# Kernel tuning notes

Measured on AMD Instinct MI355X. Metric: run time of the kernel, lower is better.

The kernel has to match this reference:

```python
import jax, jax.numpy as jnp
import numpy as np

B, T = 1024, 128
LEN_VOCAB, IPD_VOCAB = 1500, 256
LEN_EB, IPD_EB = 64, 64
RNN_IN, HIDDEN, LABELS = 128, 512, 100


def setup_inputs() -> dict:
    key = jax.random.key(0)
    ks = jax.random.split(key, 11)
    std = 1.0 / np.sqrt(HIDDEN)

    def u(k, shape, s):
        return jax.random.uniform(k, shape, jnp.float32, -s, s)

    return {
        "x": jax.random.randint(ks[0], (B, T, 2), 0, 256, dtype=jnp.int64),
        "len_emb": jax.random.normal(ks[1], (LEN_VOCAB, LEN_EB), jnp.float32),
        "ipd_emb": jax.random.normal(ks[2], (IPD_VOCAB, IPD_EB), jnp.float32),
        "fc1_w": u(ks[3], (RNN_IN, LEN_EB + IPD_EB), 1.0 / np.sqrt(LEN_EB + IPD_EB)),
        "fc1_b": u(ks[4], (RNN_IN,), 1.0 / np.sqrt(LEN_EB + IPD_EB)),
        "x2h_w": u(ks[5], (HIDDEN, RNN_IN), std),
        "x2h_b": u(ks[6], (HIDDEN,), std),
        "h2h_w": u(ks[7], (HIDDEN, HIDDEN), std),
        "h2h_b": u(ks[8], (HIDDEN,), std),
        "fc2_w": u(ks[9], (LABELS, HIDDEN), 1.0 / np.sqrt(HIDDEN)),
        "fc2_b": u(ks[10], (LABELS,), 1.0 / np.sqrt(HIDDEN)),
    }


def reference(x, len_emb, ipd_emb, fc1_w, fc1_b, x2h_w, x2h_b, h2h_w, h2h_b, fc2_w, fc2_b):
    # Embedding lookups: [B, T, 64] each -> concat [B, T, 128]
    feats = jnp.concatenate([len_emb[x[:, :, 0]], ipd_emb[x[:, :, 1]]], axis=-1)
    # fc1 then precompute the x2h part of the recurrence for all timesteps
    r = feats @ fc1_w.T + fc1_b                       # [B, T, RNN_IN]
    xin = r @ x2h_w.T + x2h_b                         # [B, T, HIDDEN]
    xin_t = jnp.swapaxes(xin, 0, 1)                   # [T, B, HIDDEN]

    def step(h, xt):
        h = jnp.tanh(xt + h @ h2h_w.T + h2h_b)
        return h, None

    h0 = jnp.zeros((x.shape[0], h2h_w.shape[0]), dtype=xin.dtype)
    h_last, _ = jax.lax.scan(step, h0, xin_t)
    # eval mode: dropout is identity
    return h_last @ fc2_w.T + fc2_b                   # [B, LABELS]
```

## Files before the change

### kernel.cpp

```cpp
#include <hip/hip_runtime.h>

#define B_SZ 1024
#define T_SZ 128
#define HID 512
#define LAB 100

#define OFF_XC    0u
#define OFF_WH    262144u
#define OFF_FC2   786432u
#define OFF_FC2B  888832u
#define OFF_WEFFT 889344u
#define OFF_BEFF  1151488u
#define OFF_ELEN  1153536u
#define OFF_EIPD  1415680u
#define WS_NEED   1677824u

typedef __attribute__((ext_vector_type(8))) short short8;
typedef __attribute__((ext_vector_type(8))) unsigned short us8;
typedef __attribute__((ext_vector_type(4))) float float4v;
typedef __attribute__((ext_vector_type(4))) unsigned short us4;
typedef __attribute__((ext_vector_type(8))) __bf16 bf8_t;
typedef unsigned long long ull;

__device__ __attribute__((aligned(16))) unsigned char g_blob[WS_NEED];

__device__ __forceinline__ float bf2f(unsigned short u) {
    union { unsigned int i; float f; } z; z.i = ((unsigned int)u) << 16; return z.f;
}
__device__ __forceinline__ unsigned short f2bf(float f) {
    union { float f; unsigned int i; } z; z.f = f;
    unsigned int r = z.i + 0x7FFFu + ((z.i >> 16) & 1u);
    return (unsigned short)(r >> 16);
}
__device__ __forceinline__ float4v mfma16(short8 a, short8 b, float4v c) {
    return __builtin_amdgcn_mfma_f32_16x16x32_bf16(
        __builtin_bit_cast(bf8_t, a), __builtin_bit_cast(bf8_t, b), c, 0, 0, 0);
}

__launch_bounds__(256)
__global__ void k1_kernel(const float* __restrict__ fc1_f, const float* __restrict__ fc1b_f,
                          const float* __restrict__ x2h_f, const float* __restrict__ x2hb_f,
                          const float* __restrict__ h2hb_f,
                          float* __restrict__ wefft, float* __restrict__ beff) {
    const int tid = threadIdx.x;
    if (blockIdx.x < 64) {
        int gid = blockIdx.x * 256 + tid;
        int n  = gid >> 5;
        int k0 = (gid & 31) * 4;
        const float* xr = x2h_f + n * 128;
        float a0 = 0.f, a1 = 0.f, a2 = 0.f, a3 = 0.f;
#pragma unroll 4
        for (int j = 0; j < 128; j++) {
            float xv = xr[j];
            float4v fv = *(const float4v*)(fc1_f + j * 128 + k0);
            a0 += xv * fv[0]; a1 += xv * fv[1];
            a2 += xv * fv[2]; a3 += xv * fv[3];
        }
        wefft[(k0 + 0) * 512 + n] = a0;
        wefft[(k0 + 1) * 512 + n] = a1;
        wefft[(k0 + 2) * 512 + n] = a2;
        wefft[(k0 + 3) * 512 + n] = a3;
        return;
    }
    int tg = (blockIdx.x - 64) * 256 + tid;
    float s = x2hb_f[tg] + h2hb_f[tg];
    const float4v* xr = (const float4v*)(x2h_f + tg * 128);
    const float4v* bb = (const float4v*)fc1b_f;
    for (int j = 0; j < 32; j++) {
        float4v a = xr[j], b = bb[j];
        s += a[0] * b[0] + a[1] * b[1] + a[2] * b[2] + a[3] * b[3];
    }
    beff[tg] = s;
}

__launch_bounds__(256)
__global__ void k2_kernel(const float* __restrict__ wefft, const float* __restrict__ beff,
                          const float* __restrict__ len_f, const float* __restrict__ ipd_f,
                          const int* __restrict__ xi, unsigned char* __restrict__ xc,
                          const float* __restrict__ h2h_f, const float* __restrict__ fc2_f,
                          const float* __restrict__ fc2b_f,
                          unsigned short* __restrict__ elen, unsigned short* __restrict__ eipd,
                          unsigned short* __restrict__ o_wh, unsigned short* __restrict__ o_fc2,
                          float* __restrict__ o_fc2b) {
    const int tid = threadIdx.x;
    if (blockIdx.x < 256) {
        int grp = blockIdx.x * 256 + tid;
        int tab = grp >> 15;
        int g2  = grp & 32767;
        int v   = g2 >> 7;
        int nq  = (g2 & 127) * 4;
        const float* emb = (tab ? ipd_f : len_f) + v * 64;
        const float* wt  = wefft + tab * 64 * 512 + nq;
        float a0 = 0.f, a1 = 0.f, a2 = 0.f, a3 = 0.f;
#pragma unroll 8
        for (int k = 0; k < 64; k++) {
            float e = emb[k];
            float4v w = *(const float4v*)(wt + k * 512);
            a0 += e * w[0]; a1 += e * w[1]; a2 += e * w[2]; a3 += e * w[3];
        }
        if (tab) {
            float4v b4 = *(const float4v*)&beff[nq];
            a0 += b4[0]; a1 += b4[1]; a2 += b4[2]; a3 += b4[3];
        }
        int nt = (nq >> 4) & 3, qq = (nq >> 2) & 3;
        int p0 = (nq & ~63) + ((nt >> 1) << 5) + qq * 8 + ((nt & 1) << 2);
        us4 o = { f2bf(a0), f2bf(a1), f2bf(a2), f2bf(a3) };
        unsigned short* dst = tab ? eipd : elen;
        *(us4*)&dst[v * 512 + p0] = o;
        return;
    }
    if (blockIdx.x < 512) {
        __shared__ int is64;
        if (tid == 0) {
            int nz = 0;
            for (int j = 1; j < 64; j += 2) nz |= xi[j];
            is64 = (nz == 0) ? 1 : 0;
        }
        __syncthreads();
        const int n = B_SZ * T_SZ * 2;
        const int i64 = is64;
        for (int i = (blockIdx.x - 256) * 256 + tid; i < n; i += 256 * 256) {
            int v = i64 ? xi[2 * i] : xi[i];
            v = v < 0 ? 0 : (v > 255 ? 255 : v);
            int b = i >> 8, r = i & 255, t = r >> 1, c = r & 1;
            xc[t * 2048 + b * 2 + c] = (unsigned char)v;
        }
        return;
    }
    const int N2 = 262144, N3 = 51200, N5 = 100;
    const int total = N2 + N3 + N5;
    for (int i = (blockIdx.x - 512) * 256 + tid; i < total; i += 613 * 256) {
        int j = i;
        if (j < N2) { o_wh[j] = f2bf(h2h_f[j]); continue; }
        j -= N2;
        if (j < N3) { o_fc2[j] = f2bf(fc2_f[j]); continue; }
        j -= N3;
        o_fc2b[j] = fc2b_f[j];
    }
}

__launch_bounds__(512, 2)
__global__ void rnn_kernel(const unsigned short* __restrict__ w_wh,
                           const unsigned char* __restrict__ w_xc,
                           const unsigned short* __restrict__ w_elen,
                           const unsigned short* __restrict__ w_eipd,
                           const unsigned short* __restrict__ w_fc2,
                           const float* __restrict__ w_fc2b,
                           float* __restrict__ out) {
    extern __shared__ unsigned short sm2[];
    unsigned short* sA = sm2;
    unsigned short* sH = sm2 + 65536;

    const int tid  = threadIdx.x;
    const int wv   = tid >> 6;
    const int ln   = tid & 63;
    const int mcol = ln & 15;
    const int q    = ln >> 4;
    const int g    = blockIdx.x;
    const int b0   = g * 16;
    const int n0   = wv * 64;

    for (int it = 0; it < 16; it++) {
        int chunk = it * 512 + tid;
        int r = chunk >> 4, c = chunk & 15;
        uint4 v = *(const uint4*)(w_wh + r * 512 + 384 + c * 8);
        *(uint4*)&sA[r * 128 + ((c ^ (r & 15)) & 15) * 8] = v;
    }
    {
        uint4 z = {0, 0, 0, 0};
        *(uint4*)&sH[tid * 8] = z;
        *(uint4*)&sH[(512 + tid) * 8] = z;
    }
    short8 whr[4][12];
#pragma unroll
    for (int nt = 0; nt < 4; nt++)
#pragma unroll
        for (int kt = 0; kt < 12; kt++)
            whr[nt][kt] = *(const short8*)(w_wh + (n0 + nt * 16 + mcol) * 512 + kt * 32 + q * 8);

    const int qlo = (q ^ (mcol & 3)) * 8;
    int ej[4];
#pragma unroll
    for (int j = 0; j < 4; j++)
        ej[j] = ((j * 4) ^ (mcol & 12)) * 8;
    const int base_b = mcol * 512 + qlo;
    const int fbase  = (n0 + mcol) * 128 + qlo;
    int hw_off[4];
#pragma unroll
    for (int nt = 0; nt < 4; nt++) {
        int n = n0 + nt * 16 + q * 4;
        hw_off[nt] = mcol * 512 + (((n >> 3) ^ mcol) & 63) * 8 + (n & 7);
    }

    const int xb2  = (b0 + mcol) * 2;
    const int ecol = n0 + q * 8;
    us8 tL0, tL1, tI0, tI1;
    {
        unsigned int i0 = *(const unsigned short*)&w_xc[xb2];
        const unsigned short* eL = w_elen + (i0 & 255u) * 512 + ecol;
        const unsigned short* eI = w_eipd + (i0 >> 8) * 512 + ecol;
        tL0 = *(const us8*)eL;  tL1 = *(const us8*)(eL + 32);
        tI0 = *(const us8*)eI;  tI1 = *(const us8*)(eI + 32);
    }
    unsigned int idxP = *(const unsigned short*)&w_xc[2048 + xb2];

    __syncthreads();

    for (int t = 0; t < T_SZ; t++) {
        const unsigned short* hRd = sH + ((t & 1) << 13);
        unsigned short* hWr = sH + (((t + 1) & 1) << 13);

        float4v acc[4];
#pragma unroll
        for (int r = 0; r < 4; r++) {
            acc[0][r] = bf2f(tL0[r])     + bf2f(tI0[r]);
            acc[1][r] = bf2f(tL0[4 + r]) + bf2f(tI0[4 + r]);
            acc[2][r] = bf2f(tL1[r])     + bf2f(tI1[r]);
            acc[3][r] = bf2f(tL1[4 + r]) + bf2f(tI1[4 + r]);
        }
        if (t + 1 < T_SZ) {
            const unsigned short* eL = w_elen + (idxP & 255u) * 512 + ecol;
            const unsigned short* eI = w_eipd + (idxP >> 8) * 512 + ecol;
            tL0 = *(const us8*)eL;  tL1 = *(const us8*)(eL + 32);
            tI0 = *(const us8*)eI;  tI1 = *(const us8*)(eI + 32);
            if (t + 2 < T_SZ)
                idxP = *(const unsigned short*)&w_xc[(t + 2) * 2048 + xb2];
        }

#pragma unroll
        for (int kt = 0; kt < 12; kt++) {
            short8 bh = *(const short8*)&hRd[base_b + ej[kt & 3] + (kt >> 2) * 128];
#pragma unroll
            for (int nt = 0; nt < 4; nt++)
                acc[nt] = mfma16(whr[nt][kt], bh, acc[nt]);
        }
#pragma unroll
        for (int j = 0; j < 4; j++) {
            short8 bh = *(const short8*)&hRd[base_b + ej[j] + 384];
#pragma unroll
            for (int nt = 0; nt < 4; nt++) {
                short8 fa = *(const short8*)&sA[fbase + nt * 2048 + ej[j]];
                acc[nt] = mfma16(fa, bh, acc[nt]);
            }
        }

#pragma unroll
        for (int nt = 0; nt < 4; nt++) {
            unsigned short o[4];
#pragma unroll
            for (int r = 0; r < 4; r++) {
                float e  = __expf(2.0f * acc[nt][r]);
                float th = 1.0f - 2.0f * __builtin_amdgcn_rcpf(e + 1.0f);
                o[r] = f2bf(th);
            }
            us4 v4 = { o[0], o[1], o[2], o[3] };
            *(us4*)&hWr[hw_off[nt]] = v4;
        }
        __syncthreads();
    }

    unsigned short* hF = sH;

    if (wv < 7) {
        int lA = wv * 16 + mcol; if (lA > 99) lA = 99;
        float4v a2 = {0.f, 0.f, 0.f, 0.f};
#pragma unroll
        for (int kt = 0; kt < 16; kt++) {
            short8 fa = *(const short8*)(w_fc2 + lA * 512 + kt * 32 + q * 8);
            short8 bh = *(const short8*)&hF[base_b + ej[kt & 3] + (kt >> 2) * 128];
            a2 = mfma16(fa, bh, a2);
        }
#pragma unroll
        for (int r = 0; r < 4; r++) {
            int l = wv * 16 + q * 4 + r;
            if (l < 100) out[(b0 + mcol) * 100 + l] = a2[r] + w_fc2b[l];
        }
    }
}

extern "C" void kernel_launch(void* const* d_in, const int* in_sizes, int n_in,
                              void* d_out, int out_size, void* d_ws, size_t ws_size,
                              hipStream_t stream) {
    unsigned char* base = (unsigned char*)d_ws;
    if (ws_size < (size_t)WS_NEED) {
        void* p = nullptr;
        hipGetSymbolAddress(&p, HIP_SYMBOL(g_blob));
        base = (unsigned char*)p;
    }
    unsigned char*  w_xc    = base + OFF_XC;
    unsigned short* w_wh    = (unsigned short*)(base + OFF_WH);
    unsigned short* w_fc2   = (unsigned short*)(base + OFF_FC2);
    float*          w_fc2b  = (float*)(base + OFF_FC2B);
    float*          w_wefft = (float*)(base + OFF_WEFFT);
    float*          w_beff  = (float*)(base + OFF_BEFF);
    unsigned short* w_elen  = (unsigned short*)(base + OFF_ELEN);
    unsigned short* w_eipd  = (unsigned short*)(base + OFF_EIPD);

    static bool attr_set = false;
    if (!attr_set) {
        hipFuncSetAttribute((const void*)rnn_kernel,
                            hipFuncAttributeMaxDynamicSharedMemorySize, 163840);
        attr_set = true;
    }

    k1_kernel<<<66, 256, 0, stream>>>(
        (const float*)d_in[3], (const float*)d_in[4],
        (const float*)d_in[5], (const float*)d_in[6], (const float*)d_in[8],
        w_wefft, w_beff);
    k2_kernel<<<1125, 256, 0, stream>>>(
        w_wefft, w_beff,
        (const float*)d_in[1], (const float*)d_in[2],
        (const int*)d_in[0], w_xc,
        (const float*)d_in[7], (const float*)d_in[9], (const float*)d_in[10],
        w_elen, w_eipd, w_wh, w_fc2, w_fc2b);
    rnn_kernel<<<64, 512, 163840, stream>>>(
        w_wh, w_xc, w_elen, w_eipd, w_fc2, w_fc2b, (float*)d_out);
}
```

Before: 354.8 us.

## Fuse prep kernels with flag sync and keep more h2h weights in registers

Result: slower. 488.8 us (+37.8%).

```diff
diff --git a/kernel.cpp b/kernel.cpp
--- a/kernel.cpp
+++ b/kernel.cpp
@@ -13,7 +13,8 @@
 #define OFF_BEFF  1151488u
 #define OFF_ELEN  1153536u
 #define OFF_EIPD  1415680u
-#define WS_NEED   1677824u
+#define OFF_FLAGS 1677824u
+#define WS_NEED   1677840u
 
 typedef __attribute__((ext_vector_type(8))) short short8;
 typedef __attribute__((ext_vector_type(8))) unsigned short us8;
@@ -38,13 +39,22 @@
 }
 
 __launch_bounds__(256)
-__global__ void k1_kernel(const float* __restrict__ fc1_f, const float* __restrict__ fc1b_f,
-                          const float* __restrict__ x2h_f, const float* __restrict__ x2hb_f,
-                          const float* __restrict__ h2hb_f,
-                          float* __restrict__ wefft, float* __restrict__ beff) {
+__global__ void k12_kernel(const float* __restrict__ fc1_f, const float* __restrict__ fc1b_f,
+                           const float* __restrict__ x2h_f, const float* __restrict__ x2hb_f,
+                           const float* __restrict__ h2hb_f,
+                           const float* __restrict__ len_f, const float* __restrict__ ipd_f,
+                           const int* __restrict__ xi, unsigned char* __restrict__ xc,
+                           const float* __restrict__ h2h_f, const float* __restrict__ fc2_f,
+                           const float* __restrict__ fc2b_f,
+                           float* wefft, float* beff,
+                           unsigned short* __restrict__ elen, unsigned short* __restrict__ eipd,
+                           unsigned short* __restrict__ o_wh, unsigned short* __restrict__ o_fc2,
+                           float* __restrict__ o_fc2b,
+                           unsigned int* __restrict__ flags) {
     const int tid = threadIdx.x;
-    if (blockIdx.x < 64) {
-        int gid = blockIdx.x * 256 + tid;
+    const int b   = blockIdx.x;
+    if (b < 64) {
+        int gid = b * 256 + tid;
         int n  = gid >> 5;
         int k0 = (gid & 31) * 4;
         const float* xr = x2h_f + n * 128;
@@ -60,31 +70,38 @@
         wefft[(k0 + 1) * 512 + n] = a1;
         wefft[(k0 + 2) * 512 + n] = a2;
         wefft[(k0 + 3) * 512 + n] = a3;
+        __syncthreads();
+        if (tid == 0) {
+            __threadfence();
+            __hip_atomic_fetch_add(&flags[0], 1u, __ATOMIC_RELEASE, __HIP_MEMORY_SCOPE_SYSTEM);
+        }
         return;
     }
-    int tg = (blockIdx.x - 64) * 256 + tid;
-    float s = x2hb_f[tg] + h2hb_f[tg];
-    const float4v* xr = (const float4v*)(x2h_f + tg * 128);
-    const float4v* bb = (const float4v*)fc1b_f;
-    for (int j = 0; j < 32; j++) {
-        float4v a = xr[j], b = bb[j];
-        s += a[0] * b[0] + a[1] * b[1] + a[2] * b[2] + a[3] * b[3];
-    }
-    beff[tg] = s;
-}
-
-__launch_bounds__(256)
-__global__ void k2_kernel(const float* __restrict__ wefft, const float* __restrict__ beff,
-                          const float* __restrict__ len_f, const float* __restrict__ ipd_f,
-                          const int* __restrict__ xi, unsigned char* __restrict__ xc,
-                          const float* __restrict__ h2h_f, const float* __restrict__ fc2_f,
-                          const float* __restrict__ fc2b_f,
-                          unsigned short* __restrict__ elen, unsigned short* __restrict__ eipd,
-                          unsigned short* __restrict__ o_wh, unsigned short* __restrict__ o_fc2,
-                          float* __restrict__ o_fc2b) {
-    const int tid = threadIdx.x;
-    if (blockIdx.x < 256) {
-        int grp = blockIdx.x * 256 + tid;
+    if (b < 66) {
+        int tg = (b - 64) * 256 + tid;
+        float s = x2hb_f[tg] + h2hb_f[tg];
+        const float4v* xr = (const float4v*)(x2h_f + tg * 128);
+        const float4v* bb = (const float4v*)fc1b_f;
+        for (int j = 0; j < 32; j++) {
+            float4v a = xr[j], c = bb[j];
+            s += a[0] * c[0] + a[1] * c[1] + a[2] * c[2] + a[3] * c[3];
+        }
+        beff[tg] = s;
+        __syncthreads();
+        if (tid == 0) {
+            __threadfence();
+            __hip_atomic_fetch_add(&flags[0], 1u, __ATOMIC_RELEASE, __HIP_MEMORY_SCOPE_SYSTEM);
+        }
+        return;
+    }
+    if (b < 322) {
+        if (tid == 0) {
+            while (__hip_atomic_load(&flags[0], __ATOMIC_RELAXED, __HIP_MEMORY_SCOPE_SYSTEM) < 66u)
+                __builtin_amdgcn_s_sleep(8);
+            __threadfence();
+        }
+        __syncthreads();
+        int grp = (b - 66) * 256 + tid;
         int tab = grp >> 15;
         int g2  = grp & 32767;
         int v   = g2 >> 7;
@@ -109,7 +126,7 @@
         *(us4*)&dst[v * 512 + p0] = o;
         return;
     }
-    if (blockIdx.x < 512) {
+    if (b < 578) {
         __shared__ int is64;
         if (tid == 0) {
             int nz = 0;
@@ -119,17 +136,17 @@
         __syncthreads();
         const int n = B_SZ * T_SZ * 2;
         const int i64 = is64;
-        for (int i = (blockIdx.x - 256) * 256 + tid; i < n; i += 256 * 256) {
+        for (int i = (b - 322) * 256 + tid; i < n; i += 256 * 256) {
             int v = i64 ? xi[2 * i] : xi[i];
             v = v < 0 ? 0 : (v > 255 ? 255 : v);
-            int b = i >> 8, r = i & 255, t = r >> 1, c = r & 1;
-            xc[t * 2048 + b * 2 + c] = (unsigned char)v;
+            int bb2 = i >> 8, r = i & 255, t = r >> 1, c = r & 1;
+            xc[t * 2048 + bb2 * 2 + c] = (unsigned char)v;
         }
         return;
     }
     const int N2 = 262144, N3 = 51200, N5 = 100;
     const int total = N2 + N3 + N5;
-    for (int i = (blockIdx.x - 512) * 256 + tid; i < total; i += 613 * 256) {
+    for (int i = (b - 578) * 256 + tid; i < total; i += 613 * 256) {
         int j = i;
         if (j < N2) { o_wh[j] = f2bf(h2h_f[j]); continue; }
         j -= N2;
@@ -149,7 +166,7 @@
                            float* __restrict__ out) {
     extern __shared__ unsigned short sm2[];
     unsigned short* sA = sm2;
-    unsigned short* sH = sm2 + 65536;
+    unsigned short* sH = sm2 + 32768;
 
     const int tid  = threadIdx.x;
     const int wv   = tid >> 6;
@@ -160,22 +177,22 @@
     const int b0   = g * 16;
     const int n0   = wv * 64;
 
-    for (int it = 0; it < 16; it++) {
+    for (int it = 0; it < 8; it++) {
         int chunk = it * 512 + tid;
-        int r = chunk >> 4, c = chunk & 15;
-        uint4 v = *(const uint4*)(w_wh + r * 512 + 384 + c * 8);
-        *(uint4*)&sA[r * 128 + ((c ^ (r & 15)) & 15) * 8] = v;
+        int r = chunk >> 3, c = chunk & 7;
+        uint4 v = *(const uint4*)(w_wh + r * 512 + 448 + c * 8);
+        *(uint4*)&sA[r * 64 + ((c ^ (r & 7)) & 7) * 8] = v;
     }
     {
         uint4 z = {0, 0, 0, 0};
         *(uint4*)&sH[tid * 8] = z;
         *(uint4*)&sH[(512 + tid) * 8] = z;
     }
-    short8 whr[4][12];
+    short8 whr[4][14];
 #pragma unroll
     for (int nt = 0; nt < 4; nt++)
 #pragma unroll
-        for (int kt = 0; kt < 12; kt++)
+        for (int kt = 0; kt < 14; kt++)
             whr[nt][kt] = *(const short8*)(w_wh + (n0 + nt * 16 + mcol) * 512 + kt * 32 + q * 8);
 
     const int qlo = (q ^ (mcol & 3)) * 8;
@@ -183,8 +200,12 @@
 #pragma unroll
     for (int j = 0; j < 4; j++)
         ej[j] = ((j * 4) ^ (mcol & 12)) * 8;
+    int ej2[2];
+#pragma unroll
+    for (int j = 0; j < 2; j++)
+        ej2[j] = ((j * 4) ^ (mcol & 4)) * 8;
     const int base_b = mcol * 512 + qlo;
-    const int fbase  = (n0 + mcol) * 128 + qlo;
+    const int fbase  = (n0 + mcol) * 64 + qlo;
     int hw_off[4];
 #pragma unroll
     for (int nt = 0; nt < 4; nt++) {
@@ -228,18 +249,18 @@
         }
 
 #pragma unroll
-        for (int kt = 0; kt < 12; kt++) {
+        for (int kt = 0; kt < 14; kt++) {
             short8 bh = *(const short8*)&hRd[base_b + ej[kt & 3] + (kt >> 2) * 128];
 #pragma unroll
             for (int nt = 0; nt < 4; nt++)
                 acc[nt] = mfma16(whr[nt][kt], bh, acc[nt]);
         }
 #pragma unroll
-        for (int j = 0; j < 4; j++) {
-            short8 bh = *(const short8*)&hRd[base_b + ej[j] + 384];
+        for (int j = 0; j < 2; j++) {
+            short8 bh = *(const short8*)&hRd[base_b + ej[2 + j] + 384];
 #pragma unroll
             for (int nt = 0; nt < 4; nt++) {
-                short8 fa = *(const short8*)&sA[fbase + nt * 2048 + ej[j]];
+                short8 fa = *(const short8*)&sA[fbase + nt * 1024 + ej2[j]];
                 acc[nt] = mfma16(fa, bh, acc[nt]);
             }
         }
@@ -295,24 +316,24 @@
     float*          w_beff  = (float*)(base + OFF_BEFF);
     unsigned short* w_elen  = (unsigned short*)(base + OFF_ELEN);
     unsigned short* w_eipd  = (unsigned short*)(base + OFF_EIPD);
+    unsigned int*   w_flags = (unsigned int*)(base + OFF_FLAGS);
 
     static bool attr_set = false;
     if (!attr_set) {
         hipFuncSetAttribute((const void*)rnn_kernel,
-                            hipFuncAttributeMaxDynamicSharedMemorySize, 163840);
+                            hipFuncAttributeMaxDynamicSharedMemorySize, 98304);
         attr_set = true;
     }
 
-    k1_kernel<<<66, 256, 0, stream>>>(
+    hipMemsetAsync(w_flags, 0, 16, stream);
+    k12_kernel<<<1191, 256, 0, stream>>>(
         (const float*)d_in[3], (const float*)d_in[4],
         (const float*)d_in[5], (const float*)d_in[6], (const float*)d_in[8],
-        w_wefft, w_beff);
-    k2_kernel<<<1125, 256, 0, stream>>>(
-        w_wefft, w_beff,
         (const float*)d_in[1], (const float*)d_in[2],
         (const int*)d_in[0], w_xc,
         (const float*)d_in[7], (const float*)d_in[9], (const float*)d_in[10],
-        w_elen, w_eipd, w_wh, w_fc2, w_fc2b);
-    rnn_kernel<<<64, 512, 163840, stream>>>(
+        w_wefft, w_beff, w_elen, w_eipd, w_wh, w_fc2, w_fc2b,
+        w_flags);
+    rnn_kernel<<<64, 512, 98304, stream>>>(
         w_wh, w_xc, w_elen, w_eipd, w_fc2, w_fc2b, (float*)d_out);
 }
```

## Restructure prep kernels and overlap embedding-table build with RNN prologue via flags

Applied to the files above, without the earlier changes.

After: 440.3 us. +24.1%, slower.

```diff
diff --git a/kernel.cpp b/kernel.cpp
--- a/kernel.cpp
+++ b/kernel.cpp
@@ -13,7 +13,8 @@
 #define OFF_BEFF  1151488u
 #define OFF_ELEN  1153536u
 #define OFF_EIPD  1415680u
-#define WS_NEED   1677824u
+#define OFF_FLAGS 1677824u
+#define WS_NEED   1677840u
 
 typedef __attribute__((ext_vector_type(8))) short short8;
 typedef __attribute__((ext_vector_type(8))) unsigned short us8;
@@ -38,13 +39,19 @@
 }
 
 __launch_bounds__(256)
-__global__ void k1_kernel(const float* __restrict__ fc1_f, const float* __restrict__ fc1b_f,
+__global__ void k0_kernel(const float* __restrict__ fc1_f, const float* __restrict__ fc1b_f,
                           const float* __restrict__ x2h_f, const float* __restrict__ x2hb_f,
                           const float* __restrict__ h2hb_f,
-                          float* __restrict__ wefft, float* __restrict__ beff) {
+                          const int* __restrict__ xi, unsigned char* __restrict__ xc,
+                          const float* __restrict__ h2h_f, const float* __restrict__ fc2_f,
+                          const float* __restrict__ fc2b_f,
+                          float* __restrict__ wefft, float* __restrict__ beff,
+                          unsigned short* __restrict__ o_wh, unsigned short* __restrict__ o_fc2,
+                          float* __restrict__ o_fc2b) {
     const int tid = threadIdx.x;
-    if (blockIdx.x < 64) {
-        int gid = blockIdx.x * 256 + tid;
+    const int b   = blockIdx.x;
+    if (b < 64) {
+        int gid = b * 256 + tid;
         int n  = gid >> 5;
         int k0 = (gid & 31) * 4;
         const float* xr = x2h_f + n * 128;
@@ -62,29 +69,64 @@
         wefft[(k0 + 3) * 512 + n] = a3;
         return;
     }
-    int tg = (blockIdx.x - 64) * 256 + tid;
-    float s = x2hb_f[tg] + h2hb_f[tg];
-    const float4v* xr = (const float4v*)(x2h_f + tg * 128);
-    const float4v* bb = (const float4v*)fc1b_f;
-    for (int j = 0; j < 32; j++) {
-        float4v a = xr[j], b = bb[j];
-        s += a[0] * b[0] + a[1] * b[1] + a[2] * b[2] + a[3] * b[3];
-    }
-    beff[tg] = s;
-}
-
-__launch_bounds__(256)
-__global__ void k2_kernel(const float* __restrict__ wefft, const float* __restrict__ beff,
-                          const float* __restrict__ len_f, const float* __restrict__ ipd_f,
-                          const int* __restrict__ xi, unsigned char* __restrict__ xc,
-                          const float* __restrict__ h2h_f, const float* __restrict__ fc2_f,
-                          const float* __restrict__ fc2b_f,
-                          unsigned short* __restrict__ elen, unsigned short* __restrict__ eipd,
-                          unsigned short* __restrict__ o_wh, unsigned short* __restrict__ o_fc2,
-                          float* __restrict__ o_fc2b) {
+    if (b < 66) {
+        int tg = (b - 64) * 256 + tid;
+        float s = x2hb_f[tg] + h2hb_f[tg];
+        const float4v* xr = (const float4v*)(x2h_f + tg * 128);
+        const float4v* bb = (const float4v*)fc1b_f;
+        for (int j = 0; j < 32; j++) {
+            float4v a = xr[j], c = bb[j];
+            s += a[0] * c[0] + a[1] * c[1] + a[2] * c[2] + a[3] * c[3];
+        }
+        beff[tg] = s;
+        return;
+    }
+    if (b < 322) {
+        __shared__ int is64;
+        if (tid == 0) {
+            int nz = 0;
+            for (int j = 1; j < 64; j += 2) nz |= xi[j];
+            is64 = (nz == 0) ? 1 : 0;
+        }
+        __syncthreads();
+        const int n = B_SZ * T_SZ * 2;
+        const int i64 = is64;
+        for (int i = (b - 66) * 256 + tid; i < n; i += 256 * 256) {
+            int v = i64 ? xi[2 * i] : xi[i];
+            v = v < 0 ? 0 : (v > 255 ? 255 : v);
+            int bb2 = i >> 8, r = i & 255, t = r >> 1, c = r & 1;
+            xc[t * 2048 + bb2 * 2 + c] = (unsigned char)v;
+        }
+        return;
+    }
+    const int N2 = 262144, N3 = 51200, N5 = 100;
+    const int total = N2 + N3 + N5;
+    for (int i = (b - 322) * 256 + tid; i < total; i += 613 * 256) {
+        int j = i;
+        if (j < N2) { o_wh[j] = f2bf(h2h_f[j]); continue; }
+        j -= N2;
+        if (j < N3) { o_fc2[j] = f2bf(fc2_f[j]); continue; }
+        j -= N3;
+        o_fc2b[j] = fc2b_f[j];
+    }
+}
+
+__launch_bounds__(512, 2)
+__global__ void fused_kernel(const float* __restrict__ wefft, const float* __restrict__ beff,
+                             const float* __restrict__ len_f, const float* __restrict__ ipd_f,
+                             unsigned short* __restrict__ elen, unsigned short* __restrict__ eipd,
+                             const unsigned short* __restrict__ w_wh,
+                             const unsigned char* __restrict__ w_xc,
+                             const unsigned short* __restrict__ w_fc2,
+                             const float* __restrict__ w_fc2b,
+                             unsigned int* __restrict__ flags,
+                             float* __restrict__ out) {
+    extern __shared__ unsigned short sm2[];
     const int tid = threadIdx.x;
-    if (blockIdx.x < 256) {
-        int grp = blockIdx.x * 256 + tid;
+    const int b   = blockIdx.x;
+
+    if (b < 128) {
+        int grp = b * 512 + tid;
         int tab = grp >> 15;
         int g2  = grp & 32767;
         int v   = g2 >> 7;
@@ -107,56 +149,22 @@
         us4 o = { f2bf(a0), f2bf(a1), f2bf(a2), f2bf(a3) };
         unsigned short* dst = tab ? eipd : elen;
         *(us4*)&dst[v * 512 + p0] = o;
+        __syncthreads();
+        if (tid == 0) {
+            __threadfence();
+            __hip_atomic_fetch_add(&flags[0], 1u, __ATOMIC_RELEASE, __HIP_MEMORY_SCOPE_SYSTEM);
+        }
         return;
     }
-    if (blockIdx.x < 512) {
-        __shared__ int is64;
-        if (tid == 0) {
-            int nz = 0;
-            for (int j = 1; j < 64; j += 2) nz |= xi[j];
-            is64 = (nz == 0) ? 1 : 0;
-        }
-        __syncthreads();
-        const int n = B_SZ * T_SZ * 2;
-        const int i64 = is64;
-        for (int i = (blockIdx.x - 256) * 256 + tid; i < n; i += 256 * 256) {
-            int v = i64 ? xi[2 * i] : xi[i];
-            v = v < 0 ? 0 : (v > 255 ? 255 : v);
-            int b = i >> 8, r = i & 255, t = r >> 1, c = r & 1;
-            xc[t * 2048 + b * 2 + c] = (unsigned char)v;
-        }
-        return;
-    }
-    const int N2 = 262144, N3 = 51200, N5 = 100;
-    const int total = N2 + N3 + N5;
-    for (int i = (blockIdx.x - 512) * 256 + tid; i < total; i += 613 * 256) {
-        int j = i;
-        if (j < N2) { o_wh[j] = f2bf(h2h_f[j]); continue; }
-        j -= N2;
-        if (j < N3) { o_fc2[j] = f2bf(fc2_f[j]); continue; }
-        j -= N3;
-        o_fc2b[j] = fc2b_f[j];
-    }
-}
-
-__launch_bounds__(512, 2)
-__global__ void rnn_kernel(const unsigned short* __restrict__ w_wh,
-                           const unsigned char* __restrict__ w_xc,
-                           const unsigned short* __restrict__ w_elen,
-                           const unsigned short* __restrict__ w_eipd,
-                           const unsigned short* __restrict__ w_fc2,
-                           const float* __restrict__ w_fc2b,
-                           float* __restrict__ out) {
-    extern __shared__ unsigned short sm2[];
+
     unsigned short* sA = sm2;
     unsigned short* sH = sm2 + 65536;
 
-    const int tid  = threadIdx.x;
     const int wv   = tid >> 6;
     const int ln   = tid & 63;
     const int mcol = ln & 15;
     const int q    = ln >> 4;
-    const int g    = blockIdx.x;
+    const int g    = b - 128;
     const int b0   = g * 16;
     const int n0   = wv * 64;
 
@@ -192,13 +200,20 @@
         hw_off[nt] = mcol * 512 + (((n >> 3) ^ mcol) & 63) * 8 + (n & 7);
     }
 
+    if (tid == 0) {
+        while (__hip_atomic_load(&flags[0], __ATOMIC_RELAXED, __HIP_MEMORY_SCOPE_SYSTEM) < 128u)
+            __builtin_amdgcn_s_sleep(8);
+        __threadfence();
+    }
+    __syncthreads();
+
     const int xb2  = (b0 + mcol) * 2;
     const int ecol = n0 + q * 8;
     us8 tL0, tL1, tI0, tI1;
     {
         unsigned int i0 = *(const unsigned short*)&w_xc[xb2];
-        const unsigned short* eL = w_elen + (i0 & 255u) * 512 + ecol;
-        const unsigned short* eI = w_eipd + (i0 >> 8) * 512 + ecol;
+        const unsigned short* eL = elen + (i0 & 255u) * 512 + ecol;
+        const unsigned short* eI = eipd + (i0 >> 8) * 512 + ecol;
         tL0 = *(const us8*)eL;  tL1 = *(const us8*)(eL + 32);
         tI0 = *(const us8*)eI;  tI1 = *(const us8*)(eI + 32);
     }
@@ -219,8 +234,8 @@
             acc[3][r] = bf2f(tL1[4 + r]) + bf2f(tI1[4 + r]);
         }
         if (t + 1 < T_SZ) {
-            const unsigned short* eL = w_elen + (idxP & 255u) * 512 + ecol;
-            const unsigned short* eI = w_eipd + (idxP >> 8) * 512 + ecol;
+            const unsigned short* eL = elen + (idxP & 255u) * 512 + ecol;
+            const unsigned short* eI = eipd + (idxP >> 8) * 512 + ecol;
             tL0 = *(const us8*)eL;  tL1 = *(const us8*)(eL + 32);
             tI0 = *(const us8*)eI;  tI1 = *(const us8*)(eI + 32);
             if (t + 2 < T_SZ)
@@ -295,24 +310,26 @@
     float*          w_beff  = (float*)(base + OFF_BEFF);
     unsigned short* w_elen  = (unsigned short*)(base + OFF_ELEN);
     unsigned short* w_eipd  = (unsigned short*)(base + OFF_EIPD);
+    unsigned int*   w_flags = (unsigned int*)(base + OFF_FLAGS);
 
     static bool attr_set = false;
     if (!attr_set) {
-        hipFuncSetAttribute((const void*)rnn_kernel,
+        hipFuncSetAttribute((const void*)fused_kernel,
                             hipFuncAttributeMaxDynamicSharedMemorySize, 163840);
         attr_set = true;
     }
 
-    k1_kernel<<<66, 256, 0, stream>>>(
+    hipMemsetAsync(w_flags, 0, 16, stream);
+    k0_kernel<<<935, 256, 0, stream>>>(
         (const float*)d_in[3], (const float*)d_in[4],
         (const float*)d_in[5], (const float*)d_in[6], (const float*)d_in[8],
-        w_wefft, w_beff);
-    k2_kernel<<<1125, 256, 0, stream>>>(
+        (const int*)d_in[0], w_xc,
+        (const float*)d_in[7], (const float*)d_in[9], (const float*)d_in[10],
+        w_wefft, w_beff, w_wh, w_fc2, w_fc2b);
+    fused_kernel<<<192, 512, 163840, stream>>>(
         w_wefft, w_beff,
         (const float*)d_in[1], (const float*)d_in[2],
-        (const int*)d_in[0], w_xc,
-        (const float*)d_in[7], (const float*)d_in[9], (const float*)d_in[10],
-        w_elen, w_eipd, w_wh, w_fc2, w_fc2b);
-    rnn_kernel<<<64, 512, 163840, stream>>>(
-        w_wh, w_xc, w_elen, w_eipd, w_fc2, w_fc2b, (float*)d_out);
-}
+        w_elen, w_eipd,
+        w_wh, w_xc, w_fc2, w_fc2b,
+        w_flags, (float*)d_out);
+}
```
